# Optimization experiments

Measured on AMD Instinct MI355X. Metric: run time of the kernel, lower is better.

## Reference

```python
import jax, jax.numpy as jnp
from jax import lax
import numpy as np

N_QUBITS = 10  # min(dim, n_wires) wires carry RX gates; rest stay |0>


def setup_inputs() -> dict:
    key = jax.random.key(0)
    k1, k2, k3, k4 = jax.random.split(key, 4)
    T, B, D, H, C = 128, 512, 512, 512, 32
    inputs = jax.random.normal(k1, (T, B, D), dtype=jnp.float32)
    # 4 gates (f, i, g, o), centres init ~ 0.1 * randn as in the module
    centres = 0.1 * jax.random.normal(k2, (4, C, D + H), dtype=jnp.float32)
    lin_w = jax.random.normal(k3, (4, H, C), dtype=jnp.float32) / jnp.sqrt(jnp.float32(C))
    lin_b = jax.random.normal(k4, (4, H), dtype=jnp.float32) * 0.01
    return {"inputs": inputs, "centres": centres, "lin_w": lin_w, "lin_b": lin_b}


def _quantum_kernel(comb, ctr):
    # comb: [B, dim], ctr: [C, dim]
    # Circuit = RX(x_i) then RX(-y_i) on wire i (i < N_QUBITS) => RX(x_i - y_i).
    # |<0..0|state>| = prod_i |cos((x_i - y_i)/2)| over active wires.
    m = min(comb.shape[-1], N_QUBITS)
    diff = comb[:, None, :m] - ctr[None, :, :m]  # [B, C, m]
    return jnp.prod(jnp.abs(jnp.cos(0.5 * diff)), axis=-1)  # [B, C]


def reference(inputs, centres, lin_w, lin_b):
    T, B, D = inputs.shape
    H = lin_w.shape[1]
    h0 = jnp.zeros((B, H), dtype=inputs.dtype)
    c0 = jnp.zeros((B, H), dtype=inputs.dtype)

    def step(carry, x):
        h, c = carry
        comb = jnp.concatenate([x, h], axis=1)  # [B, D+H]
        # kernels for all 4 gates at once: [4, B, C]
        k = jax.vmap(lambda ct: _quantum_kernel(comb, ct))(centres)
        pre = jnp.einsum('gbc,ghc->gbh', k, lin_w) + lin_b[:, None, :]  # [4, B, H]
        f = jax.nn.sigmoid(pre[0])
        i = jax.nn.sigmoid(pre[1])
        g = jnp.tanh(pre[2])
        o = jax.nn.sigmoid(pre[3])
        c_new = f * c + i * g
        h_new = o * jnp.tanh(c_new)
        return (h_new, c_new), h_new

    (h, c), outputs = lax.scan(step, (h0, c0), inputs)
    return outputs, h, c
```

## Files before the change

kernel.cpp:

```cpp
#include <hip/hip_runtime.h>

#define TT 128
#define BB 512
#define DD 512
#define HH 512
#define CC 32
#define NQ 10
#define GC 128
#define DH 1024
#define CHUNK 8
#define NCHUNK (TT / CHUNK)
#define L2E 1.4426950408889634f

typedef __fp16 h2 __attribute__((ext_vector_type(2)));
typedef __fp16 h4 __attribute__((ext_vector_type(4)));
typedef __fp16 h8 __attribute__((ext_vector_type(8)));
typedef float f4 __attribute__((ext_vector_type(4)));

__device__ __forceinline__ float rcpf(float x) { return __builtin_amdgcn_rcpf(x); }
__device__ __forceinline__ float exp2fast(float x) {
#if __has_builtin(__builtin_amdgcn_exp2f)
    return __builtin_amdgcn_exp2f(x);
#else
    return exp2f(x);
#endif
}

__global__ __launch_bounds__(512, 2) void qlstm_kernel(
    const float* __restrict__ inputs,
    const float* __restrict__ centres,
    const float* __restrict__ lin_w,
    const float* __restrict__ lin_b,
    float* __restrict__ out)
{
    __shared__ __fp16 Klds[TT * GC];
    __shared__ __align__(16) uint2 preB[8 * HH];
    __shared__ float blds[4 * HH];

    float* csT = (float*)preB;
    float* xsA = (float*)preB + NQ * 128;

    const int b = blockIdx.x;
    const int tid = threadIdx.x;
    const int lane = tid & 63;
    const int w = tid >> 6;
    const int q = lane >> 4;
    const int c16 = lane & 15;

    for (int idx = tid; idx < TT * NQ; idx += 512) {
        int t = idx / NQ, d = idx - t * NQ;
        xsA[t * 12 + d] = 0.5f * inputs[((size_t)t * BB + b) * DD + d];
    }
    for (int idx = tid; idx < GC * NQ; idx += 512) {
        int gc = idx & 127, d = idx >> 7;
        csT[d * 128 + gc] = 0.5f * centres[(size_t)gc * DH + d];
    }
    for (int idx = tid; idx < 4 * HH; idx += 512) {
        int g = idx >> 9;
        float s = (g == 2) ? (2.f * L2E) : (-L2E);
        blds[idx] = s * lin_b[idx];
    }
    __syncthreads();

    h8 bfr[16];
    {
        const int c0 = q * 8;
        #pragma unroll
        for (int g = 0; g < 4; ++g) {
            const float s = (g == 2) ? (2.f * L2E) : (-L2E);
            #pragma unroll
            for (int j = 0; j < 4; ++j) {
                const int hcol = (w * 4 + j) * 16 + c16;
                const float* wp = lin_w + (((size_t)g * HH + hcol) * CC + c0);
                f4 lo = *(const f4*)wp;
                f4 hi = *(const f4*)(wp + 4);
                h2 p0 = __builtin_amdgcn_cvt_pkrtz(s * lo.x, s * lo.y);
                h2 p1 = __builtin_amdgcn_cvt_pkrtz(s * lo.z, s * lo.w);
                h2 p2 = __builtin_amdgcn_cvt_pkrtz(s * hi.x, s * hi.y);
                h2 p3 = __builtin_amdgcn_cvt_pkrtz(s * hi.z, s * hi.w);
                h8 bb = { p0.x, p0.y, p1.x, p1.y, p2.x, p2.y, p3.x, p3.y };
                bfr[g * 4 + j] = bb;
            }
        }
    }

    {
        const int gcq = (tid & 31) * 4;
        const int t0 = tid >> 5;
        #pragma unroll
        for (int p = 0; p < 8; ++p) {
            const int t = t0 + p * 16;
            float pr0 = 1.f, pr1 = 1.f, pr2 = 1.f, pr3 = 1.f;
            #pragma unroll
            for (int d = 0; d < NQ; ++d) {
                float xd = xsA[t * 12 + d];
                f4 cd = *(const f4*)&csT[d * 128 + gcq];
                pr0 *= fabsf(__cosf(xd - cd.x));
                pr1 *= fabsf(__cosf(xd - cd.y));
                pr2 *= fabsf(__cosf(xd - cd.z));
                pr3 *= fabsf(__cosf(xd - cd.w));
            }
            h2 lo2 = __builtin_amdgcn_cvt_pkrtz(pr0, pr1);
            h2 hi2 = __builtin_amdgcn_cvt_pkrtz(pr2, pr3);
            h4 kk = { lo2.x, lo2.y, hi2.x, hi2.y };
            int byteo = (t * 256 + gcq * 2) ^ ((t & 7) << 4);
            *(h4*)((char*)Klds + byteo) = kk;
        }
    }
    __syncthreads();

    float cs2 = 0.f, hstate = 0.f;
    float* op = out + (size_t)b * HH + tid;
    const int tlo = c16 & 7;
    int aoff[4];
    #pragma unroll
    for (int g = 0; g < 4; ++g)
        aoff[g] = tlo * 256 + ((g * 64 + q * 16) ^ (tlo << 4));
    const int hcolbase = w * 64 + c16;

    for (int ct = 0; ct < NCHUNK; ++ct) {
        const char* arp = (const char*)Klds + ct * 2048;
        h8 afr[4];
        #pragma unroll
        for (int g = 0; g < 4; ++g)
            afr[g] = *(const h8*)(arp + aoff[g]);

        #pragma unroll
        for (int j = 0; j < 4; ++j) {
            const int hcol = hcolbase + j * 16;
            const float bf = blds[0 * HH + hcol];
            const float bi = blds[1 * HH + hcol];
            const float bg = blds[2 * HH + hcol];
            const float bo = blds[3 * HH + hcol];
            f4 cf = { bf, bf, bf, bf };
            f4 ci = { bi, bi, bi, bi };
            f4 cg = { bg, bg, bg, bg };
            f4 co = { bo, bo, bo, bo };
            f4 aF = __builtin_amdgcn_mfma_f32_16x16x32_f16(afr[0], bfr[0*4+j], cf, 0, 0, 0);
            f4 aI = __builtin_amdgcn_mfma_f32_16x16x32_f16(afr[1], bfr[1*4+j], ci, 0, 0, 0);
            f4 aG = __builtin_amdgcn_mfma_f32_16x16x32_f16(afr[2], bfr[2*4+j], cg, 0, 0, 0);
            f4 aO = __builtin_amdgcn_mfma_f32_16x16x32_f16(afr[3], bfr[3*4+j], co, 0, 0, 0);
            if (q < 2) {
                #pragma unroll
                for (int r = 0; r < 4; ++r) {
                    float F   = rcpf(1.f + exp2fast(aF[r]));
                    float si  = rcpf(1.f + exp2fast(aI[r]));
                    float rg  = rcpf(1.f + exp2fast(aG[r]));
                    float gg2 = fmaf(-4.f * L2E, rg, 2.f * L2E);
                    float O   = rcpf(1.f + exp2fast(aO[r]));
                    h2 io = __builtin_amdgcn_cvt_pkrtz(si * gg2, O);
                    uint2 uu;
                    uu.x = __builtin_bit_cast(unsigned, F);
                    uu.y = *(unsigned*)&io;
                    preB[(q * 4 + r) * HH + hcol] = uu;
                }
            }
        }

        #pragma unroll
        for (int s = 0; s < CHUNK; ++s) {
            uint2 vv = preB[s * HH + tid];
            float F = __builtin_bit_cast(float, vv.x);
            h2 io = *(h2*)&vv.y;
            cs2 = fmaf(F, cs2, (float)io.x);
            float th = fmaf(-2.f, rcpf(1.f + exp2fast(cs2)), 1.f);
            hstate = (float)io.y * th;
            op[(size_t)(ct * CHUNK + s) * (BB * HH)] = hstate;
        }
    }

    float* hout = out + (size_t)TT * BB * HH;
    float* cout = hout + (size_t)BB * HH;
    hout[(size_t)b * HH + tid] = hstate;
    cout[(size_t)b * HH + tid] = cs2 * 0.34657359027997264f;
}

extern "C" void kernel_launch(void* const* d_in, const int* in_sizes, int n_in,
                              void* d_out, int out_size, void* d_ws, size_t ws_size,
                              hipStream_t stream) {
    const float* inputs  = (const float*)d_in[0];
    const float* centres = (const float*)d_in[1];
    const float* lin_w   = (const float*)d_in[2];
    const float* lin_b   = (const float*)d_in[3];
    float* out = (float*)d_out;

    qlstm_kernel<<<dim3(BB), dim3(512), 0, stream>>>(inputs, centres, lin_w, lin_b, out);
}
```

Baseline: 101.5 us.

## Split hidden dimension across two blocks and balance gate activations across lanes

Each batch row is now handled by two 256-thread blocks, each owning half of the hidden units, doubling the grid and raising blocks per CU via launch bounds. Each block still builds the full quantum-kernel table, so the cosine work is duplicated. Gate activations are now split across all four lane quads: the low half computes forget/output and the high half computes input/cell. This replaces the old scheme where half the lanes sat idle. The forget gate is now stored in fp16 rather than fp32, which slightly lowers precision in the cell-state recurrence.

```diff
diff --git a/kernel.cpp b/kernel.cpp
--- a/kernel.cpp
+++ b/kernel.cpp
@@ -10,6 +10,7 @@
 #define DH 1024
 #define CHUNK 8
 #define NCHUNK (TT / CHUNK)
+#define HLOC 256
 #define L2E 1.4426950408889634f
 
 typedef __fp16 h2 __attribute__((ext_vector_type(2)));
@@ -26,7 +27,7 @@
 #endif
 }
 
-__global__ __launch_bounds__(512, 2) void qlstm_kernel(
+__global__ __launch_bounds__(256, 3) void qlstm_kernel(
     const float* __restrict__ inputs,
     const float* __restrict__ centres,
     const float* __restrict__ lin_w,
@@ -34,31 +35,35 @@
     float* __restrict__ out)
 {
     __shared__ __fp16 Klds[TT * GC];
-    __shared__ __align__(16) uint2 preB[8 * HH];
-    __shared__ float blds[4 * HH];
+    __shared__ __align__(16) unsigned preBx[CHUNK * HLOC * 2];
+    __shared__ float blds[4 * HLOC];
 
-    float* csT = (float*)preB;
-    float* xsA = (float*)preB + NQ * 128;
+    float* csT = (float*)preBx;
+    float* xsA = (float*)preBx + NQ * 128;
 
-    const int b = blockIdx.x;
+    const int bid = blockIdx.x;
+    const int b = bid >> 1;
+    const int hbase = (bid & 1) * HLOC;
+
     const int tid = threadIdx.x;
     const int lane = tid & 63;
     const int w = tid >> 6;
     const int q = lane >> 4;
     const int c16 = lane & 15;
+    const int hi = lane >> 5;
 
-    for (int idx = tid; idx < TT * NQ; idx += 512) {
+    for (int idx = tid; idx < TT * NQ; idx += 256) {
         int t = idx / NQ, d = idx - t * NQ;
         xsA[t * 12 + d] = 0.5f * inputs[((size_t)t * BB + b) * DD + d];
     }
-    for (int idx = tid; idx < GC * NQ; idx += 512) {
+    for (int idx = tid; idx < GC * NQ; idx += 256) {
         int gc = idx & 127, d = idx >> 7;
         csT[d * 128 + gc] = 0.5f * centres[(size_t)gc * DH + d];
     }
-    for (int idx = tid; idx < 4 * HH; idx += 512) {
-        int g = idx >> 9;
+    for (int idx = tid; idx < 4 * HLOC; idx += 256) {
+        int g = idx >> 8, hl = idx & 255;
         float s = (g == 2) ? (2.f * L2E) : (-L2E);
-        blds[idx] = s * lin_b[idx];
+        blds[idx] = s * lin_b[g * HH + hbase + hl];
     }
     __syncthreads();
 
@@ -70,14 +75,14 @@
             const float s = (g == 2) ? (2.f * L2E) : (-L2E);
             #pragma unroll
             for (int j = 0; j < 4; ++j) {
-                const int hcol = (w * 4 + j) * 16 + c16;
-                const float* wp = lin_w + (((size_t)g * HH + hcol) * CC + c0);
+                const int hcolg = hbase + w * 64 + j * 16 + c16;
+                const float* wp = lin_w + (((size_t)g * HH + hcolg) * CC + c0);
                 f4 lo = *(const f4*)wp;
-                f4 hi = *(const f4*)(wp + 4);
+                f4 hif = *(const f4*)(wp + 4);
                 h2 p0 = __builtin_amdgcn_cvt_pkrtz(s * lo.x, s * lo.y);
                 h2 p1 = __builtin_amdgcn_cvt_pkrtz(s * lo.z, s * lo.w);
-                h2 p2 = __builtin_amdgcn_cvt_pkrtz(s * hi.x, s * hi.y);
-                h2 p3 = __builtin_amdgcn_cvt_pkrtz(s * hi.z, s * hi.w);
+                h2 p2 = __builtin_amdgcn_cvt_pkrtz(s * hif.x, s * hif.y);
+                h2 p3 = __builtin_amdgcn_cvt_pkrtz(s * hif.z, s * hif.w);
                 h8 bb = { p0.x, p0.y, p1.x, p1.y, p2.x, p2.y, p3.x, p3.y };
                 bfr[g * 4 + j] = bb;
             }
@@ -88,8 +93,8 @@
         const int gcq = (tid & 31) * 4;
         const int t0 = tid >> 5;
         #pragma unroll
-        for (int p = 0; p < 8; ++p) {
-            const int t = t0 + p * 16;
+        for (int p = 0; p < 16; ++p) {
+            const int t = t0 + p * 8;
             float pr0 = 1.f, pr1 = 1.f, pr2 = 1.f, pr3 = 1.f;
             #pragma unroll
             for (int d = 0; d < NQ; ++d) {
@@ -110,13 +115,14 @@
     __syncthreads();
 
     float cs2 = 0.f, hstate = 0.f;
-    float* op = out + (size_t)b * HH + tid;
+    float* op = out + (size_t)b * HH + hbase + tid;
     const int tlo = c16 & 7;
     int aoff[4];
     #pragma unroll
     for (int g = 0; g < 4; ++g)
         aoff[g] = tlo * 256 + ((g * 64 + q * 16) ^ (tlo << 4));
-    const int hcolbase = w * 64 + c16;
+    const int hclbase = w * 64 + c16;
+    const int rl0 = (q & 1) * 4;
 
     for (int ct = 0; ct < NCHUNK; ++ct) {
         const char* arp = (const char*)Klds + ct * 2048;
@@ -127,11 +133,11 @@
 
         #pragma unroll
         for (int j = 0; j < 4; ++j) {
-            const int hcol = hcolbase + j * 16;
-            const float bf = blds[0 * HH + hcol];
-            const float bi = blds[1 * HH + hcol];
-            const float bg = blds[2 * HH + hcol];
-            const float bo = blds[3 * HH + hcol];
+            const int hcl = hclbase + j * 16;
+            const float bf = blds[0 * HLOC + hcl];
+            const float bi = blds[1 * HLOC + hcl];
+            const float bg = blds[2 * HLOC + hcl];
+            const float bo = blds[3 * HLOC + hcl];
             f4 cf = { bf, bf, bf, bf };
             f4 ci = { bi, bi, bi, bi };
             f4 cg = { bg, bg, bg, bg };
@@ -140,39 +146,39 @@
             f4 aI = __builtin_amdgcn_mfma_f32_16x16x32_f16(afr[1], bfr[1*4+j], ci, 0, 0, 0);
             f4 aG = __builtin_amdgcn_mfma_f32_16x16x32_f16(afr[2], bfr[2*4+j], cg, 0, 0, 0);
             f4 aO = __builtin_amdgcn_mfma_f32_16x16x32_f16(afr[3], bfr[3*4+j], co, 0, 0, 0);
-            if (q < 2) {
-                #pragma unroll
-                for (int r = 0; r < 4; ++r) {
-                    float F   = rcpf(1.f + exp2fast(aF[r]));
-                    float si  = rcpf(1.f + exp2fast(aI[r]));
-                    float rg  = rcpf(1.f + exp2fast(aG[r]));
-                    float gg2 = fmaf(-4.f * L2E, rg, 2.f * L2E);
-                    float O   = rcpf(1.f + exp2fast(aO[r]));
-                    h2 io = __builtin_amdgcn_cvt_pkrtz(si * gg2, O);
-                    uint2 uu;
-                    uu.x = __builtin_bit_cast(unsigned, F);
-                    uu.y = *(unsigned*)&io;
-                    preB[(q * 4 + r) * HH + hcol] = uu;
-                }
+            #pragma unroll
+            for (int r = 0; r < 4; ++r) {
+                float selA = hi ? aI[r] : aF[r];
+                float selB = hi ? aG[r] : aO[r];
+                float e1 = rcpf(1.f + exp2fast(selA));
+                float e2 = rcpf(1.f + exp2fast(selB));
+                float gg2 = fmaf(-4.f * L2E, e2, 2.f * L2E);
+                float ig2 = e1 * gg2;
+                h2 pk = __builtin_amdgcn_cvt_pkrtz(e1, e2);
+                unsigned uval = hi ? __builtin_bit_cast(unsigned, ig2)
+                                   : *(unsigned*)&pk;
+                preBx[((rl0 + r) * HLOC + hcl) * 2 + hi] = uval;
             }
         }
 
         #pragma unroll
         for (int s = 0; s < CHUNK; ++s) {
-            uint2 vv = preB[s * HH + tid];
-            float F = __builtin_bit_cast(float, vv.x);
-            h2 io = *(h2*)&vv.y;
-            cs2 = fmaf(F, cs2, (float)io.x);
+            uint2 vv = *(const uint2*)&preBx[(s * HLOC + tid) * 2];
+            h2 fo = *(h2*)&vv.x;
+            float F = (float)fo.x;
+            float O = (float)fo.y;
+            float IG2 = __builtin_bit_cast(float, vv.y);
+            cs2 = fmaf(F, cs2, IG2);
             float th = fmaf(-2.f, rcpf(1.f + exp2fast(cs2)), 1.f);
-            hstate = (float)io.y * th;
+            hstate = O * th;
             op[(size_t)(ct * CHUNK + s) * (BB * HH)] = hstate;
         }
     }
 
     float* hout = out + (size_t)TT * BB * HH;
     float* cout = hout + (size_t)BB * HH;
-    hout[(size_t)b * HH + tid] = hstate;
-    cout[(size_t)b * HH + tid] = cs2 * 0.34657359027997264f;
+    hout[(size_t)b * HH + hbase + tid] = hstate;
+    cout[(size_t)b * HH + hbase + tid] = cs2 * 0.34657359027997264f;
 }
 
 extern "C" void kernel_launch(void* const* d_in, const int* in_sizes, int n_in,
@@ -184,5 +190,5 @@
     const float* lin_b   = (const float*)d_in[3];
     float* out = (float*)d_out;
 
-    qlstm_kernel<<<dim3(BB), dim3(512), 0, stream>>>(inputs, centres, lin_w, lin_b, out);
+    qlstm_kernel<<<dim3(BB * 2), dim3(256), 0, stream>>>(inputs, centres, lin_w, lin_b, out);
 }
```

After: 93.99 us. 7.4% less time.
